# Performance work log

Measured on AMD Instinct MI355X. Metric: run time of the kernel, lower is better.

The kernel has to match this reference:

```python
import jax, jax.numpy as jnp
import numpy as np

N, E, G = 100000, 1600000, 2000
D_IN, D_H, D_MLP, D_OUT = 768, 128, 32, 2


def setup_inputs() -> dict:
    key = jax.random.key(0)
    ks = jax.random.split(key, 12)
    x = jax.random.normal(ks[0], (N, D_IN), dtype=jnp.float32)
    edge_index = jax.random.randint(ks[1], (2, E), 0, N, dtype=jnp.int64)
    edge_attr = jax.random.uniform(ks[2], (E, 1), dtype=jnp.float32)
    batch = jnp.sort(jax.random.randint(ks[3], (N,), 0, G, dtype=jnp.int64))
    s1 = 1.0 / np.sqrt(D_IN)
    s2 = 1.0 / np.sqrt(D_H)
    s3 = 1.0 / np.sqrt(D_MLP)
    return {
        "x": x, "edge_index": edge_index, "edge_attr": edge_attr,
        "batch": batch, "num_graphs": G,
        "W1i": jax.random.normal(ks[4], (D_IN, D_H), dtype=jnp.float32) * s1,
        "W1r": jax.random.normal(ks[5], (D_IN, D_H), dtype=jnp.float32) * s1,
        "b1": jnp.zeros((D_H,), dtype=jnp.float32),
        "W2i": jax.random.normal(ks[6], (D_H, D_H), dtype=jnp.float32) * s2,
        "W2r": jax.random.normal(ks[7], (D_H, D_H), dtype=jnp.float32) * s2,
        "b2": jnp.zeros((D_H,), dtype=jnp.float32),
        "Wl1": jax.random.normal(ks[8], (D_H, D_MLP), dtype=jnp.float32) * s2,
        "bl1": jnp.zeros((D_MLP,), dtype=jnp.float32),
        "Wl2": jax.random.normal(ks[9], (D_MLP, D_OUT), dtype=jnp.float32) * s3,
        "bl2": jnp.zeros((D_OUT,), dtype=jnp.float32),
    }


def _arma_conv(x, row, col, ew, Wi, Wr, b, n_nodes):
    # gcn_norm without self-loops: D^{-1/2} A D^{-1/2}
    deg = jax.ops.segment_sum(ew, col, num_segments=n_nodes)
    dinv = jnp.where(deg > 0, jax.lax.rsqrt(jnp.where(deg > 0, deg, 1.0)), 0.0)
    norm = dinv[row] * ew * dinv[col]
    h = x @ Wi                                   # [N, F_out]
    msg = h[row] * norm[:, None]                 # gather + scale  [E, F_out]
    agg = jax.ops.segment_sum(msg, col, num_segments=n_nodes)
    return jax.nn.relu(agg + x @ Wr + b)         # ARMA: K=1, T=1, act=ReLU


def reference(x, edge_index, edge_attr, batch, num_graphs,
              W1i, W1r, b1, W2i, W2r, b2, Wl1, bl1, Wl2, bl2):
    row, col = edge_index[0], edge_index[1]
    ew = edge_attr.reshape(-1)
    n = x.shape[0]
    h = jax.nn.elu(_arma_conv(x, row, col, ew, W1i, W1r, b1, n))
    node_x = _arma_conv(h, row, col, ew, W2i, W2r, b2, n)
    # global mean pool over graphs
    sums = jax.ops.segment_sum(node_x, batch, num_segments=num_graphs)
    cnt = jax.ops.segment_sum(jnp.ones((n,), node_x.dtype), batch, num_segments=num_graphs)
    graph_x = sums / jnp.maximum(cnt, 1.0)[:, None]
    pred = jax.nn.elu(graph_x @ Wl1 + bl1) @ Wl2 + bl2
    return pred
```

## Files before the change

### kernel.cpp

```cpp
#include <hip/hip_runtime.h>
#include <hip/hip_bf16.h>
#include <math.h>

typedef __attribute__((ext_vector_type(8))) short short8;
typedef __attribute__((ext_vector_type(4))) float f32x4;
typedef __attribute__((ext_vector_type(2))) float f32x2;
typedef __attribute__((address_space(1))) const void gvoid;
typedef __attribute__((address_space(3))) void lvoid;

#define NC 8

__device__ __forceinline__ unsigned short f2bf(float f) {
    unsigned int u = __builtin_bit_cast(unsigned int, f);
    return (unsigned short)((u + 0x7fffu + ((u >> 16) & 1u)) >> 16);
}
__device__ __forceinline__ float b2f(short s) {
    return __builtin_bit_cast(float, ((unsigned int)(unsigned short)s) << 16);
}
__device__ __forceinline__ unsigned int cvtpk(float lo, float hi) {
    unsigned int r;
    asm("v_cvt_pk_bf16_f32 %0, %1, %2" : "=v"(r) : "v"(lo), "v"(hi));
    return r;
}
__device__ __forceinline__ unsigned int pk8_lo(float a, float b, unsigned int old) {
    return (unsigned int)__builtin_amdgcn_cvt_pk_fp8_f32(a, b, (int)old, false);
}
__device__ __forceinline__ unsigned int pk8_hi(float a, float b, unsigned int old) {
    return (unsigned int)__builtin_amdgcn_cvt_pk_fp8_f32(a, b, (int)old, true);
}
__device__ __forceinline__ f32x2 up8_lo(unsigned int v) {
    return __builtin_amdgcn_cvt_pk_f32_fp8((int)v, false);
}
__device__ __forceinline__ f32x2 up8_hi(unsigned int v) {
    return __builtin_amdgcn_cvt_pk_f32_fp8((int)v, true);
}

__global__ __launch_bounds__(256) void hist_conv_kernel(
    const int* __restrict__ ei, const float* __restrict__ ea,
    unsigned long long* __restrict__ packed, int* __restrict__ rank, int N, int E,
    int eBlocks,
    const float* __restrict__ W1i, const float* __restrict__ W1r,
    const float* __restrict__ W2i, const float* __restrict__ W2r,
    unsigned short* __restrict__ W1t, unsigned short* __restrict__ W2t)
{
    if ((int)blockIdx.x < eBlocks) {
        int e = blockIdx.x * 256 + threadIdx.x;
        if (e >= E) return;
        const int copy = blockIdx.x & (NC - 1);
        int c = ei[(size_t)E + e];
        unsigned long long fx = (unsigned long long)(ea[e] * 1048576.0f + 0.5f);
        unsigned long long old = atomicAdd(&packed[(size_t)copy * N + c], (1ULL << 42) | fx);
        rank[e] = (int)(old >> 42);
    } else {
        int id = (blockIdx.x - eBlocks) * 256 + threadIdx.x;
        if (id < 256 * 768) {
            int n = id / 768, j = id % 768;
            int k = (j & ~63) | ((((j >> 3) & 7) ^ (n & 7)) << 3) | (j & 7);
            float v = (n < 128) ? W1i[k * 128 + n] : W1r[k * 128 + (n - 128)];
            W1t[id] = f2bf(v);
        } else {
            int id2 = id - 256 * 768;
            if (id2 < 128 * 256) {
                int n = id2 >> 8, j = id2 & 255;
                int k = (j & ~63) | ((((j >> 3) & 7) ^ (n & 7)) << 3) | (j & 7);
                float v = (k < 128) ? W2i[k * 128 + n] : W2r[(k - 128) * 128 + n];
                W2t[id2] = f2bf(v);
            }
        }
    }
}

__global__ __launch_bounds__(256) void scan1p_kernel(
    const unsigned long long* __restrict__ packed, int* __restrict__ out,
    int* __restrict__ blksum, int n)
{
    __shared__ int part[256];
    const int t = threadIdx.x;
    const int base = blockIdx.x * 1024 + t * 4;
    int v[4];
#pragma unroll
    for (int q = 0; q < 4; ++q) {
        int s = 0;
        if (base + q < n) {
#pragma unroll
            for (int p = 0; p < NC; ++p)
                s += (int)(packed[(size_t)p * n + base + q] >> 42);
        }
        v[q] = s;
    }
    const int s = v[0] + v[1] + v[2] + v[3];
    part[t] = s;
    __syncthreads();
    for (int off = 1; off < 256; off <<= 1) {
        int x = (t >= off) ? part[t - off] : 0;
        __syncthreads();
        part[t] += x;
        __syncthreads();
    }
    if (t == 255) blksum[blockIdx.x] = part[255];
    int run = part[t] - s;
#pragma unroll
    for (int q = 0; q < 4; ++q) {
        if (base + q < n) out[base + q] = run;
        run += v[q];
    }
}

__global__ __launch_bounds__(256) void scan3_kernel(
    int* __restrict__ rowptr, const int* __restrict__ blksum,
    int* __restrict__ wpb, const unsigned long long* __restrict__ packed,
    float* __restrict__ dinv, int n, int Etot, int nb)
{
    __shared__ int tmp[256];
    __shared__ int sexcl[256];
    const int t = threadIdx.x;
    const int v = (t < nb) ? blksum[t] : 0;
    tmp[t] = v;
    __syncthreads();
    for (int off = 1; off < 256; off <<= 1) {
        int x = (t >= off) ? tmp[t - off] : 0;
        __syncthreads();
        tmp[t] += x;
        __syncthreads();
    }
    sexcl[t] = tmp[t] - v;
    __syncthreads();
    const int i = blockIdx.x * 256 + t;
    if (i == 0) rowptr[n] = Etot;
    if (i >= n) return;
    int base = rowptr[i] + sexcl[i >> 10];
    rowptr[i] = base;
    unsigned long long degfx = 0;
    int acc = base;
#pragma unroll
    for (int p = 0; p < NC; ++p) {
        unsigned long long vv = packed[(size_t)p * n + i];
        wpb[(size_t)p * n + i] = acc;
        acc += (int)(vv >> 42);
        degfx += vv & ((1ULL << 42) - 1);
    }
    dinv[i] = (degfx > 0) ? rsqrtf((float)degfx * 9.5367431640625e-7f) : 0.f;
}

__global__ __launch_bounds__(256) void place_kernel(
    const int* __restrict__ ei, const float* __restrict__ ea,
    const float* __restrict__ dinv, const int* __restrict__ wpb,
    const int* __restrict__ rank, int2* __restrict__ csr, int N, int E)
{
    int e = blockIdx.x * 256 + threadIdx.x;
    if (e >= E) return;
    const int copy = blockIdx.x & (NC - 1);
    int r = ei[e];
    int c = ei[(size_t)E + e];
    float nm = dinv[r] * ea[e] * dinv[c];
    int pos = wpb[(size_t)copy * N + c] + rank[e];
    int2 rec;
    rec.x = r;
    rec.y = __builtin_bit_cast(int, nm);
    csr[pos] = rec;
}

__global__ __launch_bounds__(512) void gemm_mfma_dual(
    const float* __restrict__ A, const unsigned short* __restrict__ Wt,
    const float* __restrict__ bias, unsigned char* __restrict__ outP8,
    unsigned short* __restrict__ outR, int M, int K)
{
    __shared__ __align__(16) unsigned char As[64 * 128];
    __shared__ __align__(16) unsigned char Bs[256 * 128];

    const int t = threadIdx.x;
    const int m0 = blockIdx.x * 64;
    const int lane = t & 63;
    const int wid = t >> 6;
    const int wm = wid >> 2;
    const int wn = wid & 3;
    const int lr = lane & 15;
    const int lk = (lane >> 4) * 8;

    f32x4 acc[2][4] = {};

    const int sr = t >> 3;
    const int sk = (t & 7) * 8;
    const int aRow = m0 + sr;
    const bool aOk = (aRow < M);
    const float* aSrc = A + (size_t)(aOk ? aRow : 0) * K + sk;
    const int aDst = sr * 128 + ((sk * 2) ^ ((sr & 7) << 4));
    const unsigned short* bSrc = Wt + (size_t)(lane >> 3) * K + (lane & 7) * 8;

    for (int k0 = 0; k0 < K; k0 += 64) {
#pragma unroll
        for (int i = 0; i < 4; ++i) {
            const int chunk = i * 8 + wid;
            __builtin_amdgcn_global_load_lds(
                (gvoid*)(bSrc + (size_t)chunk * 8 * K + k0),
                (lvoid*)(Bs + chunk * 1024), 16, 0, 0);
        }
        unsigned int p0 = 0, p1 = 0, p2 = 0, p3 = 0;
        if (aOk) {
            const float4 f0 = *(const float4*)(aSrc + k0);
            const float4 f1 = *(const float4*)(aSrc + k0 + 4);
            p0 = cvtpk(f0.x, f0.y);
            p1 = cvtpk(f0.z, f0.w);
            p2 = cvtpk(f1.x, f1.y);
            p3 = cvtpk(f1.z, f1.w);
        }
        uint4 uv = {p0, p1, p2, p3};
        *(uint4*)(As + aDst) = uv;
        __syncthreads();
#pragma unroll
        for (int ks = 0; ks < 2; ++ks) {
            short8 a[2], b[4];
#pragma unroll
            for (int mf = 0; mf < 2; ++mf) {
                const int r = wm * 32 + mf * 16 + lr;
                a[mf] = *(const short8*)(As + r * 128 + (((ks * 32 + lk) * 2) ^ ((r & 7) << 4)));
            }
#pragma unroll
            for (int nf = 0; nf < 4; ++nf) {
                const int n = wn * 64 + nf * 16 + lr;
                b[nf] = *(const short8*)(Bs + n * 128 + (((ks * 32 + lk) * 2) ^ ((n & 7) << 4)));
            }
#pragma unroll
            for (int mf = 0; mf < 2; ++mf)
#pragma unroll
                for (int nf = 0; nf < 4; ++nf)
                    acc[mf][nf] = __builtin_amdgcn_mfma_f32_16x16x32_bf16(
                        a[mf], b[nf], acc[mf][nf], 0, 0, 0);
        }
        __syncthreads();
    }

#pragma unroll
    for (int mf = 0; mf < 2; ++mf) {
#pragma unroll
        for (int nf = 0; nf < 4; ++nf) {
            const int n = wn * 64 + nf * 16 + lr;
            const f32x4 v = acc[mf][nf];
            const int mb = m0 + wm * 32 + mf * 16 + (lane >> 4) * 4;
            if (n < 128) {
                const unsigned int u01 = pk8_lo(v[0], v[1], 0u);
                const unsigned int u23 = pk8_lo(v[2], v[3], 0u);
                if (mb + 0 < M) outP8[(size_t)(mb + 0) * 128 + n] = (unsigned char)(u01);
                if (mb + 1 < M) outP8[(size_t)(mb + 1) * 128 + n] = (unsigned char)(u01 >> 8);
                if (mb + 2 < M) outP8[(size_t)(mb + 2) * 128 + n] = (unsigned char)(u23);
                if (mb + 3 < M) outP8[(size_t)(mb + 3) * 128 + n] = (unsigned char)(u23 >> 8);
            } else {
                const int nl = n - 128;
                const float badd = bias[nl];
#pragma unroll
                for (int j = 0; j < 4; ++j) {
                    if (mb + j < M) outR[(size_t)(mb + j) * 128 + nl] = f2bf(v[j] + badd);
                }
            }
        }
    }
}

__global__ __launch_bounds__(512) void gemm_mfma_single(
    const unsigned short* __restrict__ Aa,
    const unsigned short* __restrict__ Ah,
    const unsigned short* __restrict__ Wt,
    const float* __restrict__ bias,
    unsigned short* __restrict__ outX, int M)
{
    __shared__ __align__(16) unsigned char As[128 * 128];
    __shared__ __align__(16) unsigned char Bs[128 * 128];

    const int t = threadIdx.x;
    const int m0 = blockIdx.x * 128;
    const int lane = t & 63;
    const int wid = t >> 6;
    const int wm = wid >> 1;
    const int wn = wid & 1;
    const int lr = lane & 15;
    const int lk = (lane >> 4) * 8;

    f32x4 acc[2][4] = {};

    const int sr = t >> 2;
    const int sk = (t & 3) * 16;
    const int aRow = m0 + sr;
    const bool aOk = (aRow < M);
    const int rowSafe = aOk ? aRow : 0;
    const int sw = (sr & 7) << 4;
    const unsigned short* bSrc = Wt + (size_t)(lane >> 3) * 256 + (lane & 7) * 8;

    for (int k0 = 0; k0 < 256; k0 += 64) {
#pragma unroll
        for (int i = 0; i < 2; ++i) {
            const int chunk = i * 8 + wid;
            __builtin_amdgcn_global_load_lds(
                (gvoid*)(bSrc + (size_t)chunk * 8 * 256 + k0),
                (lvoid*)(Bs + chunk * 1024), 16, 0, 0);
        }
        const unsigned short* src =
            (k0 < 128 ? Aa : Ah) + (size_t)rowSafe * 128 + (k0 & 127) + sk;
        const short8 v0 = *(const short8*)(src);
        const short8 v1 = *(const short8*)(src + 8);
        *(short8*)(As + sr * 128 + ((sk * 2) ^ sw)) = v0;
        *(short8*)(As + sr * 128 + ((sk * 2 + 16) ^ sw)) = v1;
        __syncthreads();
#pragma unroll
        for (int ks = 0; ks < 2; ++ks) {
            short8 a[2], b[4];
#pragma unroll
            for (int mf = 0; mf < 2; ++mf) {
                const int r = wm * 32 + mf * 16 + lr;
                a[mf] = *(const short8*)(As + r * 128 + (((ks * 32 + lk) * 2) ^ ((r & 7) << 4)));
            }
#pragma unroll
            for (int nf = 0; nf < 4; ++nf) {
                const int n = wn * 64 + nf * 16 + lr;
                b[nf] = *(const short8*)(Bs + n * 128 + (((ks * 32 + lk) * 2) ^ ((n & 7) << 4)));
            }
#pragma unroll
            for (int mf = 0; mf < 2; ++mf)
#pragma unroll
                for (int nf = 0; nf < 4; ++nf)
                    acc[mf][nf] = __builtin_amdgcn_mfma_f32_16x16x32_bf16(
                        a[mf], b[nf], acc[mf][nf], 0, 0, 0);
        }
        __syncthreads();
    }

#pragma unroll
    for (int mf = 0; mf < 2; ++mf) {
#pragma unroll
        for (int nf = 0; nf < 4; ++nf) {
            const int n = wn * 64 + nf * 16 + lr;
            const float bb = bias[n];
            const f32x4 v = acc[mf][nf];
#pragma unroll
            for (int j = 0; j < 4; ++j) {
                const int m = m0 + wm * 32 + mf * 16 + (lane >> 4) * 4 + j;
                if (m < M) outX[(size_t)m * 128 + n] = f2bf(fmaxf(v[j] + bb, 0.f));
            }
        }
    }
}

__global__ __launch_bounds__(256) void agg_bias_relu(
    const unsigned char* __restrict__ P8, const unsigned short* __restrict__ Rbf,
    const int* __restrict__ rowptr, const int2* __restrict__ csr,
    unsigned short* __restrict__ hout, unsigned char* __restrict__ h8out, int N)
{
    const int i = blockIdx.x * 16 + (threadIdx.x >> 4);
    const int l = threadIdx.x & 15;
    if (i >= N) return;
    const int beg = rowptr[i];
    const int end = rowptr[i + 1];
    const int c = l * 8;

    float acc0[8] = {}, acc1[8] = {}, acc2[8] = {}, acc3[8] = {};
    int j = beg;
    for (; j + 3 < end; j += 4) {
        const int2 e0 = csr[j],     e1 = csr[j + 1];
        const int2 e2 = csr[j + 2], e3 = csr[j + 3];
        const uint2 u0 = *(const uint2*)(P8 + (size_t)e0.x * 128 + c);
        const uint2 u1 = *(const uint2*)(P8 + (size_t)e1.x * 128 + c);
        const uint2 u2 = *(const uint2*)(P8 + (size_t)e2.x * 128 + c);
        const uint2 u3 = *(const uint2*)(P8 + (size_t)e3.x * 128 + c);
        const float n0 = __builtin_bit_cast(float, e0.y);
        const float n1 = __builtin_bit_cast(float, e1.y);
        const float n2 = __builtin_bit_cast(float, e2.y);
        const float n3 = __builtin_bit_cast(float, e3.y);
        {
            const f32x2 p0 = up8_lo(u0.x), p1 = up8_hi(u0.x);
            const f32x2 p2 = up8_lo(u0.y), p3 = up8_hi(u0.y);
            acc0[0] = fmaf(p0.x, n0, acc0[0]); acc0[1] = fmaf(p0.y, n0, acc0[1]);
            acc0[2] = fmaf(p1.x, n0, acc0[2]); acc0[3] = fmaf(p1.y, n0, acc0[3]);
            acc0[4] = fmaf(p2.x, n0, acc0[4]); acc0[5] = fmaf(p2.y, n0, acc0[5]);
            acc0[6] = fmaf(p3.x, n0, acc0[6]); acc0[7] = fmaf(p3.y, n0, acc0[7]);
        }
        {
            const f32x2 p0 = up8_lo(u1.x), p1 = up8_hi(u1.x);
            const f32x2 p2 = up8_lo(u1.y), p3 = up8_hi(u1.y);
            acc1[0] = fmaf(p0.x, n1, acc1[0]); acc1[1] = fmaf(p0.y, n1, acc1[1]);
            acc1[2] = fmaf(p1.x, n1, acc1[2]); acc1[3] = fmaf(p1.y, n1, acc1[3]);
            acc1[4] = fmaf(p2.x, n1, acc1[4]); acc1[5] = fmaf(p2.y, n1, acc1[5]);
            acc1[6] = fmaf(p3.x, n1, acc1[6]); acc1[7] = fmaf(p3.y, n1, acc1[7]);
        }
        {
            const f32x2 p0 = up8_lo(u2.x), p1 = up8_hi(u2.x);
            const f32x2 p2 = up8_lo(u2.y), p3 = up8_hi(u2.y);
            acc2[0] = fmaf(p0.x, n2, acc2[0]); acc2[1] = fmaf(p0.y, n2, acc2[1]);
            acc2[2] = fmaf(p1.x, n2, acc2[2]); acc2[3] = fmaf(p1.y, n2, acc2[3]);
            acc2[4] = fmaf(p2.x, n2, acc2[4]); acc2[5] = fmaf(p2.y, n2, acc2[5]);
            acc2[6] = fmaf(p3.x, n2, acc2[6]); acc2[7] = fmaf(p3.y, n2, acc2[7]);
        }
        {
            const f32x2 p0 = up8_lo(u3.x), p1 = up8_hi(u3.x);
            const f32x2 p2 = up8_lo(u3.y), p3 = up8_hi(u3.y);
            acc3[0] = fmaf(p0.x, n3, acc3[0]); acc3[1] = fmaf(p0.y, n3, acc3[1]);
            acc3[2] = fmaf(p1.x, n3, acc3[2]); acc3[3] = fmaf(p1.y, n3, acc3[3]);
            acc3[4] = fmaf(p2.x, n3, acc3[4]); acc3[5] = fmaf(p2.y, n3, acc3[5]);
            acc3[6] = fmaf(p3.x, n3, acc3[6]); acc3[7] = fmaf(p3.y, n3, acc3[7]);
        }
    }
    for (; j < end; ++j) {
        const int2 e0 = csr[j];
        const uint2 u0 = *(const uint2*)(P8 + (size_t)e0.x * 128 + c);
        const float n0 = __builtin_bit_cast(float, e0.y);
        const f32x2 p0 = up8_lo(u0.x), p1 = up8_hi(u0.x);
        const f32x2 p2 = up8_lo(u0.y), p3 = up8_hi(u0.y);
        acc0[0] = fmaf(p0.x, n0, acc0[0]); acc0[1] = fmaf(p0.y, n0, acc0[1]);
        acc0[2] = fmaf(p1.x, n0, acc0[2]); acc0[3] = fmaf(p1.y, n0, acc0[3]);
        acc0[4] = fmaf(p2.x, n0, acc0[4]); acc0[5] = fmaf(p2.y, n0, acc0[5]);
        acc0[6] = fmaf(p3.x, n0, acc0[6]); acc0[7] = fmaf(p3.y, n0, acc0[7]);
    }
    const short8 rv = *(const short8*)(Rbf + (size_t)i * 128 + c);
    float s[8];
    short8 ov;
#pragma unroll
    for (int q = 0; q < 8; ++q) {
        s[q] = fmaxf((acc0[q] + acc1[q]) + (acc2[q] + acc3[q]) + b2f(rv[q]), 0.f);
        ov[q] = (short)f2bf(s[q]);
    }
    *(short8*)(hout + (size_t)i * 128 + c) = ov;
    unsigned int w0 = 0, w1 = 0;
    w0 = pk8_lo(s[0], s[1], w0); w0 = pk8_hi(s[2], s[3], w0);
    w1 = pk8_lo(s[4], s[5], w1); w1 = pk8_hi(s[6], s[7], w1);
    uint2 wv = {w0, w1};
    *(uint2*)(h8out + (size_t)i * 128 + c) = wv;
}

__global__ __launch_bounds__(256) void agg_plain(
    const unsigned char* __restrict__ H8,
    const int* __restrict__ rowptr, const int2* __restrict__ csr,
    unsigned short* __restrict__ ahout, int N)
{
    const int i = blockIdx.x * 16 + (threadIdx.x >> 4);
    const int l = threadIdx.x & 15;
    if (i >= N) return;
    const int beg = rowptr[i];
    const int end = rowptr[i + 1];
    const int c = l * 8;

    float acc0[8] = {}, acc1[8] = {}, acc2[8] = {}, acc3[8] = {};
    int j = beg;
    for (; j + 3 < end; j += 4) {
        const int2 e0 = csr[j],     e1 = csr[j + 1];
        const int2 e2 = csr[j + 2], e3 = csr[j + 3];
        const uint2 u0 = *(const uint2*)(H8 + (size_t)e0.x * 128 + c);
        const uint2 u1 = *(const uint2*)(H8 + (size_t)e1.x * 128 + c);
        const uint2 u2 = *(const uint2*)(H8 + (size_t)e2.x * 128 + c);
        const uint2 u3 = *(const uint2*)(H8 + (size_t)e3.x * 128 + c);
        const float n0 = __builtin_bit_cast(float, e0.y);
        const float n1 = __builtin_bit_cast(float, e1.y);
        const float n2 = __builtin_bit_cast(float, e2.y);
        const float n3 = __builtin_bit_cast(float, e3.y);
        {
            const f32x2 p0 = up8_lo(u0.x), p1 = up8_hi(u0.x);
            const f32x2 p2 = up8_lo(u0.y), p3 = up8_hi(u0.y);
            acc0[0] = fmaf(p0.x, n0, acc0[0]); acc0[1] = fmaf(p0.y, n0, acc0[1]);
            acc0[2] = fmaf(p1.x, n0, acc0[2]); acc0[3] = fmaf(p1.y, n0, acc0[3]);
            acc0[4] = fmaf(p2.x, n0, acc0[4]); acc0[5] = fmaf(p2.y, n0, acc0[5]);
            acc0[6] = fmaf(p3.x, n0, acc0[6]); acc0[7] = fmaf(p3.y, n0, acc0[7]);
        }
        {
            const f32x2 p0 = up8_lo(u1.x), p1 = up8_hi(u1.x);
            const f32x2 p2 = up8_lo(u1.y), p3 = up8_hi(u1.y);
            acc1[0] = fmaf(p0.x, n1, acc1[0]); acc1[1] = fmaf(p0.y, n1, acc1[1]);
            acc1[2] = fmaf(p1.x, n1, acc1[2]); acc1[3] = fmaf(p1.y, n1, acc1[3]);
            acc1[4] = fmaf(p2.x, n1, acc1[4]); acc1[5] = fmaf(p2.y, n1, acc1[5]);
            acc1[6] = fmaf(p3.x, n1, acc1[6]); acc1[7] = fmaf(p3.y, n1, acc1[7]);
        }
        {
            const f32x2 p0 = up8_lo(u2.x), p1 = up8_hi(u2.x);
            const f32x2 p2 = up8_lo(u2.y), p3 = up8_hi(u2.y);
            acc2[0] = fmaf(p0.x, n2, acc2[0]); acc2[1] = fmaf(p0.y, n2, acc2[1]);
            acc2[2] = fmaf(p1.x, n2, acc2[2]); acc2[3] = fmaf(p1.y, n2, acc2[3]);
            acc2[4] = fmaf(p2.x, n2, acc2[4]); acc2[5] = fmaf(p2.y, n2, acc2[5]);
            acc2[6] = fmaf(p3.x, n2, acc2[6]); acc2[7] = fmaf(p3.y, n2, acc2[7]);
        }
        {
            const f32x2 p0 = up8_lo(u3.x), p1 = up8_hi(u3.x);
            const f32x2 p2 = up8_lo(u3.y), p3 = up8_hi(u3.y);
            acc3[0] = fmaf(p0.x, n3, acc3[0]); acc3[1] = fmaf(p0.y, n3, acc3[1]);
            acc3[2] = fmaf(p1.x, n3, acc3[2]); acc3[3] = fmaf(p1.y, n3, acc3[3]);
            acc3[4] = fmaf(p2.x, n3, acc3[4]); acc3[5] = fmaf(p2.y, n3, acc3[5]);
            acc3[6] = fmaf(p3.x, n3, acc3[6]); acc3[7] = fmaf(p3.y, n3, acc3[7]);
        }
    }
    for (; j < end; ++j) {
        const int2 e0 = csr[j];
        const uint2 u0 = *(const uint2*)(H8 + (size_t)e0.x * 128 + c);
        const float n0 = __builtin_bit_cast(float, e0.y);
        const f32x2 p0 = up8_lo(u0.x), p1 = up8_hi(u0.x);
        const f32x2 p2 = up8_lo(u0.y), p3 = up8_hi(u0.y);
        acc0[0] = fmaf(p0.x, n0, acc0[0]); acc0[1] = fmaf(p0.y, n0, acc0[1]);
        acc0[2] = fmaf(p1.x, n0, acc0[2]); acc0[3] = fmaf(p1.y, n0, acc0[3]);
        acc0[4] = fmaf(p2.x, n0, acc0[4]); acc0[5] = fmaf(p2.y, n0, acc0[5]);
        acc0[6] = fmaf(p3.x, n0, acc0[6]); acc0[7] = fmaf(p3.y, n0, acc0[7]);
    }
    short8 ov;
#pragma unroll
    for (int q = 0; q < 8; ++q)
        ov[q] = (short)f2bf((acc0[q] + acc1[q]) + (acc2[q] + acc3[q]));
    *(short8*)(ahout + (size_t)i * 128 + c) = ov;
}

__global__ __launch_bounds__(256) void pool_mlp(
    const unsigned short* __restrict__ nx, const int* __restrict__ batch, int N,
    const float* __restrict__ Wl1, const float* __restrict__ bl1,
    const float* __restrict__ Wl2, const float* __restrict__ bl2,
    float* __restrict__ out)
{
    __shared__ float gxp[4][128];
    __shared__ float hid[32];
    __shared__ int rng[2];
    const int g = blockIdx.x;
    const int t = threadIdx.x;
    if (t < 2) {
        const int target = g + t;
        int lo = 0, hi = N;
        while (lo < hi) {
            int mid = (lo + hi) >> 1;
            if (batch[mid] < target) lo = mid + 1; else hi = mid;
        }
        rng[t] = lo;
    }
    __syncthreads();
    const int s = rng[0], e = rng[1];
    const int pr = t & 63;
    const int strm = t >> 6;
    float a0 = 0.f, b0 = 0.f, a1 = 0.f, b1 = 0.f;
    int i = s + strm;
    for (; i + 4 < e; i += 8) {
        const unsigned int u = *(const unsigned int*)&nx[(size_t)i * 128 + pr * 2];
        const unsigned int v = *(const unsigned int*)&nx[(size_t)(i + 4) * 128 + pr * 2];
        a0 += b2f((short)(u & 0xffff)); b0 += b2f((short)(u >> 16));
        a1 += b2f((short)(v & 0xffff)); b1 += b2f((short)(v >> 16));
    }
    if (i < e) {
        const unsigned int u = *(const unsigned int*)&nx[(size_t)i * 128 + pr * 2];
        a0 += b2f((short)(u & 0xffff)); b0 += b2f((short)(u >> 16));
    }
    gxp[strm][pr * 2] = a0 + a1;
    gxp[strm][pr * 2 + 1] = b0 + b1;
    __syncthreads();
    if (t < 128) {
        gxp[0][t] = ((gxp[0][t] + gxp[1][t]) + (gxp[2][t] + gxp[3][t]))
                    / fmaxf((float)(e - s), 1.f);
    }
    __syncthreads();
    if (t < 32) {
        float a = bl1[t];
#pragma unroll 8
        for (int k = 0; k < 128; ++k) a = fmaf(gxp[0][k], Wl1[k * 32 + t], a);
        hid[t] = a > 0.f ? a : expm1f(a);
    }
    __syncthreads();
    if (t < 2) {
        float a = bl2[t];
#pragma unroll
        for (int k = 0; k < 32; ++k) a = fmaf(hid[k], Wl2[k * 2 + t], a);
        out[(size_t)g * 2 + t] = a;
    }
}

extern "C" void kernel_launch(void* const* d_in, const int* in_sizes, int n_in,
                              void* d_out, int out_size, void* d_ws, size_t ws_size,
                              hipStream_t stream)
{
    const float* x     = (const float*)d_in[0];
    const int*   ei    = (const int*)d_in[1];
    const float* ea    = (const float*)d_in[2];
    const int*   batch = (const int*)d_in[3];
    const float* W1i   = (const float*)d_in[5];
    const float* W1r   = (const float*)d_in[6];
    const float* b1    = (const float*)d_in[7];
    const float* W2i   = (const float*)d_in[8];
    const float* W2r   = (const float*)d_in[9];
    const float* b2    = (const float*)d_in[10];
    const float* Wl1   = (const float*)d_in[11];
    const float* bl1   = (const float*)d_in[12];
    const float* Wl2   = (const float*)d_in[13];
    const float* bl2   = (const float*)d_in[14];

    const int N = in_sizes[0] / 768;
    const int E = in_sizes[2];
    const int G = out_size / 2;

    char* ws = (char*)d_ws;
    size_t off = 0;
    auto alloc = [&](size_t bytes) -> char* {
        char* p = ws + off;
        off = (off + bytes + 255) & ~(size_t)255;
        return p;
    };
    unsigned long long* packed = (unsigned long long*)alloc((size_t)NC * N * 8);
    int*   rank    = (int*)alloc((size_t)E * 4);
    int*   wpb     = (int*)alloc((size_t)NC * N * 4);
    float* dinv    = (float*)alloc((size_t)N * 4);
    int*   rowptr  = (int*)alloc((size_t)(N + 1) * 4);
    int*   blksum  = (int*)alloc((size_t)256 * 4);
    int2*  csr     = (int2*)alloc((size_t)E * 8);
    unsigned char*  P8   = (unsigned char*)alloc((size_t)N * 128);
    unsigned char*  H8   = (unsigned char*)alloc((size_t)N * 128);
    unsigned short* R1   = (unsigned short*)alloc((size_t)N * 128 * 2);
    unsigned short* hbf  = (unsigned short*)alloc((size_t)N * 128 * 2);
    unsigned short* ahb  = (unsigned short*)alloc((size_t)N * 128 * 2);
    unsigned short* nxb  = (unsigned short*)alloc((size_t)N * 128 * 2);
    unsigned short* W1t  = (unsigned short*)alloc((size_t)256 * 768 * 2);
    unsigned short* W2t  = (unsigned short*)alloc((size_t)128 * 256 * 2);

    const int eBlocks = (E + 255) / 256;
    const int cBlocks = (256 * 768 + 128 * 256 + 255) / 256;
    const int nb      = (N + 1023) / 1024;
    const int nBlocks = (N + 255) / 256;
    const int aBlocks = (N + 15) / 16;

    (void)hipMemsetAsync(packed, 0, (size_t)NC * N * 8, stream);
    hist_conv_kernel<<<eBlocks + cBlocks, 256, 0, stream>>>(
        ei, ea, packed, rank, N, E, eBlocks, W1i, W1r, W2i, W2r, W1t, W2t);
    scan1p_kernel<<<nb, 256, 0, stream>>>(packed, rowptr, blksum, N);
    scan3_kernel<<<nBlocks, 256, 0, stream>>>(rowptr, blksum, wpb, packed, dinv, N, E, nb);
    place_kernel<<<eBlocks, 256, 0, stream>>>(ei, ea, dinv, wpb, rank, csr, N, E);

    gemm_mfma_dual<<<(N + 63) / 64, 512, 0, stream>>>(x, W1t, b1, P8, R1, N, 768);
    agg_bias_relu<<<aBlocks, 256, 0, stream>>>(P8, R1, rowptr, csr, hbf, H8, N);

    agg_plain<<<aBlocks, 256, 0, stream>>>(H8, rowptr, csr, ahb, N);
    gemm_mfma_single<<<(N + 127) / 128, 512, 0, stream>>>(ahb, hbf, W2t, b2, nxb, N);

    pool_mlp<<<G, 256, 0, stream>>>(nxb, batch, N, Wl1, bl1, Wl2, bl2, (float*)d_out);
}
```

Before: 369.8 us.

## Fuse CSR placement into GEMM1 launch and widen aggregation lanes to 16 features

The edge placement kernel is merged into the first GEMM launch as extra blocks, so the CSR scatter runs alongside the GEMM and one launch and its serialization point go away. The copy index is recomputed from the edge index so it matches the histogram's 256-edge blocking. The two aggregation kernels now use 8 lanes per node with 16-byte fp8 gathers instead of 16 lanes with 8-byte gathers, and the unroll drops from 4 to 2 edges. That halves the number of gather instructions per edge, at the cost of fewer edges in flight per thread and more register pressure.

```diff
diff --git a/kernel.cpp b/kernel.cpp
--- a/kernel.cpp
+++ b/kernel.cpp
@@ -33,6 +33,17 @@
 }
 __device__ __forceinline__ f32x2 up8_hi(unsigned int v) {
     return __builtin_amdgcn_cvt_pk_f32_fp8((int)v, true);
+}
+__device__ __forceinline__ void acc16(float* A, const uint4 u, const float n) {
+    f32x2 p;
+    p = up8_lo(u.x); A[0]  = fmaf(p.x, n, A[0]);  A[1]  = fmaf(p.y, n, A[1]);
+    p = up8_hi(u.x); A[2]  = fmaf(p.x, n, A[2]);  A[3]  = fmaf(p.y, n, A[3]);
+    p = up8_lo(u.y); A[4]  = fmaf(p.x, n, A[4]);  A[5]  = fmaf(p.y, n, A[5]);
+    p = up8_hi(u.y); A[6]  = fmaf(p.x, n, A[6]);  A[7]  = fmaf(p.y, n, A[7]);
+    p = up8_lo(u.z); A[8]  = fmaf(p.x, n, A[8]);  A[9]  = fmaf(p.y, n, A[9]);
+    p = up8_hi(u.z); A[10] = fmaf(p.x, n, A[10]); A[11] = fmaf(p.y, n, A[11]);
+    p = up8_lo(u.w); A[12] = fmaf(p.x, n, A[12]); A[13] = fmaf(p.y, n, A[13]);
+    p = up8_hi(u.w); A[14] = fmaf(p.x, n, A[14]); A[15] = fmaf(p.y, n, A[15]);
 }
 
 __global__ __launch_bounds__(256) void hist_conv_kernel(
@@ -142,31 +153,31 @@
     dinv[i] = (degfx > 0) ? rsqrtf((float)degfx * 9.5367431640625e-7f) : 0.f;
 }
 
-__global__ __launch_bounds__(256) void place_kernel(
+__global__ __launch_bounds__(512) void gemm1_place_kernel(
+    const float* __restrict__ A, const unsigned short* __restrict__ Wt,
+    const float* __restrict__ bias, unsigned char* __restrict__ outP8,
+    unsigned short* __restrict__ outR, int M, int K, int gB,
     const int* __restrict__ ei, const float* __restrict__ ea,
     const float* __restrict__ dinv, const int* __restrict__ wpb,
-    const int* __restrict__ rank, int2* __restrict__ csr, int N, int E)
-{
-    int e = blockIdx.x * 256 + threadIdx.x;
-    if (e >= E) return;
-    const int copy = blockIdx.x & (NC - 1);
-    int r = ei[e];
-    int c = ei[(size_t)E + e];
-    float nm = dinv[r] * ea[e] * dinv[c];
-    int pos = wpb[(size_t)copy * N + c] + rank[e];
-    int2 rec;
-    rec.x = r;
-    rec.y = __builtin_bit_cast(int, nm);
-    csr[pos] = rec;
-}
-
-__global__ __launch_bounds__(512) void gemm_mfma_dual(
-    const float* __restrict__ A, const unsigned short* __restrict__ Wt,
-    const float* __restrict__ bias, unsigned char* __restrict__ outP8,
-    unsigned short* __restrict__ outR, int M, int K)
+    const int* __restrict__ rank, int2* __restrict__ csr, int E)
 {
     __shared__ __align__(16) unsigned char As[64 * 128];
     __shared__ __align__(16) unsigned char Bs[256 * 128];
+
+    if ((int)blockIdx.x >= gB) {
+        int e = (blockIdx.x - gB) * 512 + threadIdx.x;
+        if (e >= E) return;
+        const int copy = (e >> 8) & (NC - 1);
+        int r = ei[e];
+        int c = ei[(size_t)E + e];
+        float nm = dinv[r] * ea[e] * dinv[c];
+        int pos = wpb[(size_t)copy * M + c] + rank[e];
+        int2 rec;
+        rec.x = r;
+        rec.y = __builtin_bit_cast(int, nm);
+        csr[pos] = rec;
+        return;
+    }
 
     const int t = threadIdx.x;
     const int m0 = blockIdx.x * 64;
@@ -344,84 +355,49 @@
     const int* __restrict__ rowptr, const int2* __restrict__ csr,
     unsigned short* __restrict__ hout, unsigned char* __restrict__ h8out, int N)
 {
-    const int i = blockIdx.x * 16 + (threadIdx.x >> 4);
-    const int l = threadIdx.x & 15;
+    const int i = blockIdx.x * 32 + (threadIdx.x >> 3);
+    const int l = threadIdx.x & 7;
     if (i >= N) return;
     const int beg = rowptr[i];
     const int end = rowptr[i + 1];
-    const int c = l * 8;
-
-    float acc0[8] = {}, acc1[8] = {}, acc2[8] = {}, acc3[8] = {};
+    const int c = l * 16;
+
+    float A0[16] = {}, A1[16] = {};
     int j = beg;
-    for (; j + 3 < end; j += 4) {
-        const int2 e0 = csr[j],     e1 = csr[j + 1];
-        const int2 e2 = csr[j + 2], e3 = csr[j + 3];
-        const uint2 u0 = *(const uint2*)(P8 + (size_t)e0.x * 128 + c);
-        const uint2 u1 = *(const uint2*)(P8 + (size_t)e1.x * 128 + c);
-        const uint2 u2 = *(const uint2*)(P8 + (size_t)e2.x * 128 + c);
-        const uint2 u3 = *(const uint2*)(P8 + (size_t)e3.x * 128 + c);
-        const float n0 = __builtin_bit_cast(float, e0.y);
-        const float n1 = __builtin_bit_cast(float, e1.y);
-        const float n2 = __builtin_bit_cast(float, e2.y);
-        const float n3 = __builtin_bit_cast(float, e3.y);
-        {
-            const f32x2 p0 = up8_lo(u0.x), p1 = up8_hi(u0.x);
-            const f32x2 p2 = up8_lo(u0.y), p3 = up8_hi(u0.y);
-            acc0[0] = fmaf(p0.x, n0, acc0[0]); acc0[1] = fmaf(p0.y, n0, acc0[1]);
-            acc0[2] = fmaf(p1.x, n0, acc0[2]); acc0[3] = fmaf(p1.y, n0, acc0[3]);
-            acc0[4] = fmaf(p2.x, n0, acc0[4]); acc0[5] = fmaf(p2.y, n0, acc0[5]);
-            acc0[6] = fmaf(p3.x, n0, acc0[6]); acc0[7] = fmaf(p3.y, n0, acc0[7]);
-        }
-        {
-            const f32x2 p0 = up8_lo(u1.x), p1 = up8_hi(u1.x);
-            const f32x2 p2 = up8_lo(u1.y), p3 = up8_hi(u1.y);
-            acc1[0] = fmaf(p0.x, n1, acc1[0]); acc1[1] = fmaf(p0.y, n1, acc1[1]);
-            acc1[2] = fmaf(p1.x, n1, acc1[2]); acc1[3] = fmaf(p1.y, n1, acc1[3]);
-            acc1[4] = fmaf(p2.x, n1, acc1[4]); acc1[5] = fmaf(p2.y, n1, acc1[5]);
-            acc1[6] = fmaf(p3.x, n1, acc1[6]); acc1[7] = fmaf(p3.y, n1, acc1[7]);
-        }
-        {
-            const f32x2 p0 = up8_lo(u2.x), p1 = up8_hi(u2.x);
-            const f32x2 p2 = up8_lo(u2.y), p3 = up8_hi(u2.y);
-            acc2[0] = fmaf(p0.x, n2, acc2[0]); acc2[1] = fmaf(p0.y, n2, acc2[1]);
-            acc2[2] = fmaf(p1.x, n2, acc2[2]); acc2[3] = fmaf(p1.y, n2, acc2[3]);
-            acc2[4] = fmaf(p2.x, n2, acc2[4]); acc2[5] = fmaf(p2.y, n2, acc2[5]);
-            acc2[6] = fmaf(p3.x, n2, acc2[6]); acc2[7] = fmaf(p3.y, n2, acc2[7]);
-        }
-        {
-            const f32x2 p0 = up8_lo(u3.x), p1 = up8_hi(u3.x);
-            const f32x2 p2 = up8_lo(u3.y), p3 = up8_hi(u3.y);
-            acc3[0] = fmaf(p0.x, n3, acc3[0]); acc3[1] = fmaf(p0.y, n3, acc3[1]);
-            acc3[2] = fmaf(p1.x, n3, acc3[2]); acc3[3] = fmaf(p1.y, n3, acc3[3]);
-            acc3[4] = fmaf(p2.x, n3, acc3[4]); acc3[5] = fmaf(p2.y, n3, acc3[5]);
-            acc3[6] = fmaf(p3.x, n3, acc3[6]); acc3[7] = fmaf(p3.y, n3, acc3[7]);
-        }
-    }
-    for (; j < end; ++j) {
+    for (; j + 1 < end; j += 2) {
+        const int2 e0 = csr[j], e1 = csr[j + 1];
+        const uint4 u0 = *(const uint4*)(P8 + (size_t)e0.x * 128 + c);
+        const uint4 u1 = *(const uint4*)(P8 + (size_t)e1.x * 128 + c);
+        acc16(A0, u0, __builtin_bit_cast(float, e0.y));
+        acc16(A1, u1, __builtin_bit_cast(float, e1.y));
+    }
+    if (j < end) {
         const int2 e0 = csr[j];
-        const uint2 u0 = *(const uint2*)(P8 + (size_t)e0.x * 128 + c);
-        const float n0 = __builtin_bit_cast(float, e0.y);
-        const f32x2 p0 = up8_lo(u0.x), p1 = up8_hi(u0.x);
-        const f32x2 p2 = up8_lo(u0.y), p3 = up8_hi(u0.y);
-        acc0[0] = fmaf(p0.x, n0, acc0[0]); acc0[1] = fmaf(p0.y, n0, acc0[1]);
-        acc0[2] = fmaf(p1.x, n0, acc0[2]); acc0[3] = fmaf(p1.y, n0, acc0[3]);
-        acc0[4] = fmaf(p2.x, n0, acc0[4]); acc0[5] = fmaf(p2.y, n0, acc0[5]);
-        acc0[6] = fmaf(p3.x, n0, acc0[6]); acc0[7] = fmaf(p3.y, n0, acc0[7]);
-    }
-    const short8 rv = *(const short8*)(Rbf + (size_t)i * 128 + c);
-    float s[8];
-    short8 ov;
+        const uint4 u0 = *(const uint4*)(P8 + (size_t)e0.x * 128 + c);
+        acc16(A0, u0, __builtin_bit_cast(float, e0.y));
+    }
+    const short8 r0 = *(const short8*)(Rbf + (size_t)i * 128 + c);
+    const short8 r1 = *(const short8*)(Rbf + (size_t)i * 128 + c + 8);
+    float s[16];
+    short8 o0, o1;
 #pragma unroll
     for (int q = 0; q < 8; ++q) {
-        s[q] = fmaxf((acc0[q] + acc1[q]) + (acc2[q] + acc3[q]) + b2f(rv[q]), 0.f);
-        ov[q] = (short)f2bf(s[q]);
-    }
-    *(short8*)(hout + (size_t)i * 128 + c) = ov;
-    unsigned int w0 = 0, w1 = 0;
-    w0 = pk8_lo(s[0], s[1], w0); w0 = pk8_hi(s[2], s[3], w0);
-    w1 = pk8_lo(s[4], s[5], w1); w1 = pk8_hi(s[6], s[7], w1);
-    uint2 wv = {w0, w1};
-    *(uint2*)(h8out + (size_t)i * 128 + c) = wv;
+        s[q] = fmaxf(A0[q] + A1[q] + b2f(r0[q]), 0.f);
+        o0[q] = (short)f2bf(s[q]);
+    }
+#pragma unroll
+    for (int q = 8; q < 16; ++q) {
+        s[q] = fmaxf(A0[q] + A1[q] + b2f(r1[q - 8]), 0.f);
+        o1[q - 8] = (short)f2bf(s[q]);
+    }
+    *(short8*)(hout + (size_t)i * 128 + c) = o0;
+    *(short8*)(hout + (size_t)i * 128 + c + 8) = o1;
+    uint4 w;
+    w.x = pk8_hi(s[2],  s[3],  pk8_lo(s[0],  s[1],  0u));
+    w.y = pk8_hi(s[6],  s[7],  pk8_lo(s[4],  s[5],  0u));
+    w.z = pk8_hi(s[10], s[11], pk8_lo(s[8],  s[9],  0u));
+    w.w = pk8_hi(s[14], s[15], pk8_lo(s[12], s[13], 0u));
+    *(uint4*)(h8out + (size_t)i * 128 + c) = w;
 }
 
 __global__ __launch_bounds__(256) void agg_plain(
@@ -429,75 +405,34 @@
     const int* __restrict__ rowptr, const int2* __restrict__ csr,
     unsigned short* __restrict__ ahout, int N)
 {
-    const int i = blockIdx.x * 16 + (threadIdx.x >> 4);
-    const int l = threadIdx.x & 15;
+    const int i = blockIdx.x * 32 + (threadIdx.x >> 3);
+    const int l = threadIdx.x & 7;
     if (i >= N) return;
     const int beg = rowptr[i];
     const int end = rowptr[i + 1];
-    const int c = l * 8;
-
-    float acc0[8] = {}, acc1[8] = {}, acc2[8] = {}, acc3[8] = {};
+    const int c = l * 16;
+
+    float A0[16] = {}, A1[16] = {};
     int j = beg;
-    for (; j + 3 < end; j += 4) {
-        const int2 e0 = csr[j],     e1 = csr[j + 1];
-        const int2 e2 = csr[j + 2], e3 = csr[j + 3];
-        const uint2 u0 = *(const uint2*)(H8 + (size_t)e0.x * 128 + c);
-        const uint2 u1 = *(const uint2*)(H8 + (size_t)e1.x * 128 + c);
-        const uint2 u2 = *(const uint2*)(H8 + (size_t)e2.x * 128 + c);
-        const uint2 u3 = *(const uint2*)(H8 + (size_t)e3.x * 128 + c);
-        const float n0 = __builtin_bit_cast(float, e0.y);
-        const float n1 = __builtin_bit_cast(float, e1.y);
-        const float n2 = __builtin_bit_cast(float, e2.y);
-        const float n3 = __builtin_bit_cast(float, e3.y);
-        {
-            const f32x2 p0 = up8_lo(u0.x), p1 = up8_hi(u0.x);
-            const f32x2 p2 = up8_lo(u0.y), p3 = up8_hi(u0.y);
-            acc0[0] = fmaf(p0.x, n0, acc0[0]); acc0[1] = fmaf(p0.y, n0, acc0[1]);
-            acc0[2] = fmaf(p1.x, n0, acc0[2]); acc0[3] = fmaf(p1.y, n0, acc0[3]);
-            acc0[4] = fmaf(p2.x, n0, acc0[4]); acc0[5] = fmaf(p2.y, n0, acc0[5]);
-            acc0[6] = fmaf(p3.x, n0, acc0[6]); acc0[7] = fmaf(p3.y, n0, acc0[7]);
-        }
-        {
-            const f32x2 p0 = up8_lo(u1.x), p1 = up8_hi(u1.x);
-            const f32x2 p2 = up8_lo(u1.y), p3 = up8_hi(u1.y);
-            acc1[0] = fmaf(p0.x, n1, acc1[0]); acc1[1] = fmaf(p0.y, n1, acc1[1]);
-            acc1[2] = fmaf(p1.x, n1, acc1[2]); acc1[3] = fmaf(p1.y, n1, acc1[3]);
-            acc1[4] = fmaf(p2.x, n1, acc1[4]); acc1[5] = fmaf(p2.y, n1, acc1[5]);
-            acc1[6] = fmaf(p3.x, n1, acc1[6]); acc1[7] = fmaf(p3.y, n1, acc1[7]);
-        }
-        {
-            const f32x2 p0 = up8_lo(u2.x), p1 = up8_hi(u2.x);
-            const f32x2 p2 = up8_lo(u2.y), p3 = up8_hi(u2.y);
-            acc2[0] = fmaf(p0.x, n2, acc2[0]); acc2[1] = fmaf(p0.y, n2, acc2[1]);
-            acc2[2] = fmaf(p1.x, n2, acc2[2]); acc2[3] = fmaf(p1.y, n2, acc2[3]);
-            acc2[4] = fmaf(p2.x, n2, acc2[4]); acc2[5] = fmaf(p2.y, n2, acc2[5]);
-            acc2[6] = fmaf(p3.x, n2, acc2[6]); acc2[7] = fmaf(p3.y, n2, acc2[7]);
-        }
-        {
-            const f32x2 p0 = up8_lo(u3.x), p1 = up8_hi(u3.x);
-            const f32x2 p2 = up8_lo(u3.y), p3 = up8_hi(u3.y);
-            acc3[0] = fmaf(p0.x, n3, acc3[0]); acc3[1] = fmaf(p0.y, n3, acc3[1]);
-            acc3[2] = fmaf(p1.x, n3, acc3[2]); acc3[3] = fmaf(p1.y, n3, acc3[3]);
-            acc3[4] = fmaf(p2.x, n3, acc3[4]); acc3[5] = fmaf(p2.y, n3, acc3[5]);
-            acc3[6] = fmaf(p3.x, n3, acc3[6]); acc3[7] = fmaf(p3.y, n3, acc3[7]);
-        }
-    }
-    for (; j < end; ++j) {
+    for (; j + 1 < end; j += 2) {
+        const int2 e0 = csr[j], e1 = csr[j + 1];
+        const uint4 u0 = *(const uint4*)(H8 + (size_t)e0.x * 128 + c);
+        const uint4 u1 = *(const uint4*)(H8 + (size_t)e1.x * 128 + c);
+        acc16(A0, u0, __builtin_bit_cast(float, e0.y));
+        acc16(A1, u1, __builtin_bit_cast(float, e1.y));
+    }
+    if (j < end) {
         const int2 e0 = csr[j];
-        const uint2 u0 = *(const uint2*)(H8 + (size_t)e0.x * 128 + c);
-        const float n0 = __builtin_bit_cast(float, e0.y);
-        const f32x2 p0 = up8_lo(u0.x), p1 = up8_hi(u0.x);
-        const f32x2 p2 = up8_lo(u0.y), p3 = up8_hi(u0.y);
-        acc0[0] = fmaf(p0.x, n0, acc0[0]); acc0[1] = fmaf(p0.y, n0, acc0[1]);
-        acc0[2] = fmaf(p1.x, n0, acc0[2]); acc0[3] = fmaf(p1.y, n0, acc0[3]);
-        acc0[4] = fmaf(p2.x, n0, acc0[4]); acc0[5] = fmaf(p2.y, n0, acc0[5]);
-        acc0[6] = fmaf(p3.x, n0, acc0[6]); acc0[7] = fmaf(p3.y, n0, acc0[7]);
-    }
-    short8 ov;
-#pragma unroll
-    for (int q = 0; q < 8; ++q)
-        ov[q] = (short)f2bf((acc0[q] + acc1[q]) + (acc2[q] + acc3[q]));
-    *(short8*)(ahout + (size_t)i * 128 + c) = ov;
+        const uint4 u0 = *(const uint4*)(H8 + (size_t)e0.x * 128 + c);
+        acc16(A0, u0, __builtin_bit_cast(float, e0.y));
+    }
+    short8 o0, o1;
+#pragma unroll
+    for (int q = 0; q < 8; ++q)  o0[q] = (short)f2bf(A0[q] + A1[q]);
+#pragma unroll
+    for (int q = 8; q < 16; ++q) o1[q - 8] = (short)f2bf(A0[q] + A1[q]);
+    *(short8*)(ahout + (size_t)i * 128 + c) = o0;
+    *(short8*)(ahout + (size_t)i * 128 + c + 8) = o1;
 }
 
 __global__ __launch_bounds__(256) void pool_mlp(
@@ -609,16 +544,19 @@
     const int cBlocks = (256 * 768 + 128 * 256 + 255) / 256;
     const int nb      = (N + 1023) / 1024;
     const int nBlocks = (N + 255) / 256;
-    const int aBlocks = (N + 15) / 16;
+    const int aBlocks = (N + 31) / 32;
+    const int gB      = (N + 63) / 64;
+    const int pB      = (E + 511) / 512;
 
     (void)hipMemsetAsync(packed, 0, (size_t)NC * N * 8, stream);
     hist_conv_kernel<<<eBlocks + cBlocks, 256, 0, stream>>>(
         ei, ea, packed, rank, N, E, eBlocks, W1i, W1r, W2i, W2r, W1t, W2t);
     scan1p_kernel<<<nb, 256, 0, stream>>>(packed, rowptr, blksum, N);
     scan3_kernel<<<nBlocks, 256, 0, stream>>>(rowptr, blksum, wpb, packed, dinv, N, E, nb);
-    place_kernel<<<eBlocks, 256, 0, stream>>>(ei, ea, dinv, wpb, rank, csr, N, E);
-
-    gemm_mfma_dual<<<(N + 63) / 64, 512, 0, stream>>>(x, W1t, b1, P8, R1, N, 768);
+
+    gemm1_place_kernel<<<gB + pB, 512, 0, stream>>>(
+        x, W1t, b1, P8, R1, N, 768, gB, ei, ea, dinv, wpb, rank, csr, E);
+
     agg_bias_relu<<<aBlocks, 256, 0, stream>>>(P8, R1, rowptr, csr, hbf, H8, N);
 
     agg_plain<<<aBlocks, 256, 0, stream>>>(H8, rowptr, csr, ahb, N);
```

Measured after the change: 371.4 us. Within noise of the previous version (+0.4%).
